# Optimization experiments

Measured on AMD Instinct MI355X. Metric: run time of the kernel, lower is better.

The kernel has to match this reference:

```python
import jax, jax.numpy as jnp
import numpy as np

B = 1024          # batch
X = 32 * 32       # x_neuron_num
Y = 16384         # y_neuron_num (codebook size)
Z = 1000          # z_neuron_num (classes)
P_BU = 0.5        # y_bottom_up_percent


def _l2n(a, axis):
    # F.normalize: x / max(||x||, 1e-12)
    return a / jnp.maximum(jnp.linalg.norm(a, axis=axis, keepdims=True), 1e-12)


def setup_inputs() -> dict:
    key = jax.random.key(0)
    ks = jax.random.split(key, 8)
    return {
        "x": jax.random.normal(ks[0], (B, 32, 32), jnp.float32),
        "z": jax.random.randint(ks[1], (B,), 0, Z),
        "x2y_w": jax.random.uniform(ks[2], (Y, X), jnp.float32),
        "z2y_w": jax.random.uniform(ks[3], (Y, Z), jnp.float32),
        "y2z_w": jax.random.uniform(ks[4], (Z, Y), jnp.float32),
        "y_age": jax.random.randint(ks[5], (1, Y), 0, 5).astype(jnp.float32),
        "z_age": jax.random.randint(ks[6], (1, Z), 0, 5).astype(jnp.float32),
        "y_threshold": jax.random.uniform(ks[7], (1, Y), jnp.float32) * 0.5,
        "per_item": 1,
    }


def reference(x, z, x2y_w, z2y_w, y2z_w, y_age, z_age, y_threshold, per_item):
    # one 'train' step (torch forward returns inside the per_item loop)
    batch = x.shape[0]
    x = _l2n(x.reshape(batch, -1), 1)                 # [B, X]
    z_hot = jax.nn.one_hot(z, Z, dtype=x.dtype)       # normalized one-hot == one-hot
    Wx = _l2n(x2y_w, 1)                               # [Y, X]
    Wz = _l2n(z2y_w, 1)                               # [Y, Z]
    U = _l2n(y2z_w, 1)                                # [Z, Y]

    y_pre = P_BU * (x @ Wx.T) + (1.0 - P_BU) * (z_hot @ Wz.T)  # [B, Y]

    age = y_age[0]
    thr = y_threshold[0]
    max_resp = jnp.max(y_pre, axis=1)                 # [B]
    max_idx = jnp.argmax(y_pre, axis=1)               # [B]
    # age/threshold tie-break: losers re-argmax over unactivated neurons
    judge = (max_resp > thr[max_idx]) | (age[max_idx] < 1.0)
    unact = (age < 1.0).astype(y_pre.dtype)           # [Y]
    any_unact = jnp.sum(unact) > 0
    fallback = jnp.argmax(y_pre * unact[None, :], axis=1)
    max_idx = jnp.where(judge | ~any_unact, max_idx, fallback)

    # --- Hebbian update of x2y / z2y, expressed as segment reductions ---
    # torch dense form: sum_b y_lr[b,j]*(inp[b]-W[j]) / divisor_j
    ones_b = jnp.ones((batch,), x.dtype)
    cnt = jax.ops.segment_sum(ones_b, max_idx, num_segments=Y)       # [Y]
    div = jnp.where(cnt > 0, cnt, 1.0)
    lr = 1.0 / (age + 1.0)                                           # [Y]
    sumx = jax.ops.segment_sum(x, max_idx, num_segments=Y)           # [Y, X]
    Wx_new = Wx + (lr[:, None] * (sumx - cnt[:, None] * Wx)) / div[:, None]
    sumz = jax.ops.segment_sum(z_hot, max_idx, num_segments=Y)       # [Y, Z]
    Wz_new = Wz + (lr[:, None] * (sumz - cnt[:, None] * Wz)) / div[:, None]
    age_new = age + cnt

    # --- threshold update: per-winner min response (3 for non-winners) ---
    seg_min = jax.ops.segment_min(max_resp, max_idx, num_segments=Y)
    y_cur = jnp.minimum(seg_min, 3.0)
    y_cur = jnp.where(y_cur > 2.0, 0.0, y_cur)
    y_lr_eff = jnp.where(cnt > 0, lr, 0.0)   # sum_b y_lr[b,j]/divisor_j
    thr_new = y_lr_eff * y_cur + (1.0 - y_lr_eff) * thr

    # --- y2z update, segmented by label z ---
    zage = z_age[0]
    zlr = 1.0 / (zage + 1.0)                                          # [Z]
    y_resp = jax.nn.one_hot(max_idx, Y, dtype=x.dtype)                # [B, Y]
    cz = jax.ops.segment_sum(ones_b, z, num_segments=Z)               # [Z]
    dz = jnp.where(cz > 0, cz, 1.0)
    sumy = jax.ops.segment_sum(y_resp, z, num_segments=Z)             # [Z, Y]
    U_new = U + (zlr[:, None] * (sumy - cz[:, None] * U)) / dz[:, None]
    zage_new = zage + cz

    y_activated_num = jnp.sum((age_new >= 1.0).astype(jnp.int32))
    return (y_activated_num, max_resp, Wx_new, Wz_new, U_new,
            thr_new[None, :], age_new[None, :], zage_new[None, :])
```

## Files before the change

### kernel.cpp

```cpp
#include <hip/hip_runtime.h>

#define B_N 1024
#define X_N 1024
#define Y_N 16384
#define Z_N 1000
#define GK  2048
#define MARGIN 0.004f

#define OFF_ACT      0
#define OFF_MAXRESP  1
#define OFF_WX       1025
#define OFF_WZ       16778241
#define OFF_U        33162241
#define OFF_THR      49546241
#define OFF_AGE      49562625
#define OFF_ZAGE     49579009

#define SCR_B_BYTES    4112ull
#define SCR_S_BYTES    67112992ull
#define SCR_A_BYTES    132648976ull
#define SCR_CAND_BYTES 136843296ull

#define WS_INV_X    0
#define WS_INV_WX   1024
#define WS_INV_WZ   17408
#define WS_FIDX     38912
#define WS_CNT      39936
#define WS_ZCNT     56320
#define WS_SEGMIN   57344
#define WS_CTR      73728
#define WS_MBITS    73736
#define WS_CCNT     74248

typedef unsigned short ushort_t;
typedef _Float16 f16x8 __attribute__((ext_vector_type(8)));
typedef float f32x4 __attribute__((ext_vector_type(4)));

__device__ __forceinline__ unsigned enc_f(float f) {
    unsigned u = __float_as_uint(f);
    return (u & 0x80000000u) ? ~u : (u | 0x80000000u);
}
__device__ __forceinline__ float dec_f(unsigned e) {
    unsigned u = (e & 0x80000000u) ? (e ^ 0x80000000u) : ~e;
    return __uint_as_float(u);
}
__device__ __forceinline__ unsigned long long pack_vi(float v, int y) {
    return ((unsigned long long)enc_f(v) << 32) |
           (unsigned long long)(0xFFFFFFFFu - (unsigned)y);
}
__device__ __forceinline__ ushort_t f2h(float f) {
    _Float16 h = (_Float16)f;
    ushort_t u; __builtin_memcpy(&u, &h, 2); return u;
}
__device__ __forceinline__ float h2f(unsigned lo16) {
    ushort_t u = (ushort_t)lo16; _Float16 h;
    __builtin_memcpy(&h, &u, 2); return (float)h;
}

#define GLOAD16(gp, lp) __builtin_amdgcn_global_load_lds( \
    (const __attribute__((address_space(1))) void*)(gp),  \
    (__attribute__((address_space(3))) void*)(lp), 16, 0, 0)

__global__ void init_kernel(int* cnt, unsigned* segmin, int* zcnt, int* ctr) {
    int i = blockIdx.x * 256 + threadIdx.x;
    if (i < Y_N) { cnt[i] = 0; segmin[i] = 0xFFFFFFFFu; }
    if (i < 1024) zcnt[i] = 0;
    if (i < 8) ctr[i] = (i == 2) ? 0x7FFFFFFF : 0;
}

__global__ void unact_kernel(const float* __restrict__ y_age, int* ctr,
                             unsigned long long* __restrict__ mbits) {
    int i = blockIdx.x * 256 + threadIdx.x;
    int a = (y_age[i] < 1.0f) ? 1 : 0;
    unsigned long long m = __ballot(a);
    int mi = a ? 0x7FFFFFFF : i;
    #pragma unroll
    for (int s = 32; s > 0; s >>= 1) mi = min(mi, __shfl_xor(mi, s, 64));
    if ((threadIdx.x & 63) == 0) {
        atomicAdd(ctr, (int)__popcll(m));
        mbits[i >> 6] = m;
        if (mi != 0x7FFFFFFF) atomicMin(&ctr[2], mi);
    }
}

__global__ __launch_bounds__(256) void pack_x_kernel(
    const float* __restrict__ x, const int* __restrict__ zlab,
    ushort_t* __restrict__ A, float* __restrict__ inv_x) {
    const int b = blockIdx.x, t = threadIdx.x;
    const int lane = t & 63, wid = t >> 6;
    float4 v = reinterpret_cast<const float4*>(x + (size_t)b * X_N)[t];
    float ss = v.x*v.x + v.y*v.y + v.z*v.z + v.w*v.w;
    #pragma unroll
    for (int s = 32; s > 0; s >>= 1) ss += __shfl_xor(ss, s, 64);
    __shared__ float red[4];
    if (lane == 0) red[wid] = ss;
    __syncthreads();
    float inv = 1.0f / fmaxf(sqrtf(red[0] + red[1] + red[2] + red[3]), 1e-12f);
    if (t == 0) inv_x[b] = inv;
    float h = 0.5f * inv;
    ushort_t o1[4] = { f2h(v.x*h), f2h(v.y*h), f2h(v.z*h), f2h(v.w*h) };
    *reinterpret_cast<uint2*>(A + (size_t)b * GK + t * 4) = *reinterpret_cast<uint2*>(o1);
    int zb = zlab[b];
    ushort_t o2[4] = { 0, 0, 0, 0 };
    int base = t * 4;
    if (zb >= base && zb < base + 4) o2[zb - base] = (ushort_t)0x3800;
    *reinterpret_cast<uint2*>(A + (size_t)b * GK + X_N + t * 4) = *reinterpret_cast<uint2*>(o2);
}

__global__ __launch_bounds__(256) void pack_w_kernel(
    const float* __restrict__ wxw, const float* __restrict__ wzw,
    ushort_t* __restrict__ Bm, float* __restrict__ inv_wx, float* __restrict__ inv_wz) {
    const int y = blockIdx.x, t = threadIdx.x;
    const int lane = t & 63, wid = t >> 6;
    float4 a = reinterpret_cast<const float4*>(wxw + (size_t)y * X_N)[t];
    float4 zv = make_float4(0.f, 0.f, 0.f, 0.f);
    if (t < 250) zv = reinterpret_cast<const float4*>(wzw + (size_t)y * Z_N)[t];
    float s1 = a.x*a.x + a.y*a.y + a.z*a.z + a.w*a.w;
    float s2 = zv.x*zv.x + zv.y*zv.y + zv.z*zv.z + zv.w*zv.w;
    #pragma unroll
    for (int s = 32; s > 0; s >>= 1) {
        s1 += __shfl_xor(s1, s, 64);
        s2 += __shfl_xor(s2, s, 64);
    }
    __shared__ float r1[4], r2[4];
    if (lane == 0) { r1[wid] = s1; r2[wid] = s2; }
    __syncthreads();
    float inv1 = 1.0f / fmaxf(sqrtf(r1[0] + r1[1] + r1[2] + r1[3]), 1e-12f);
    float inv2 = 1.0f / fmaxf(sqrtf(r2[0] + r2[1] + r2[2] + r2[3]), 1e-12f);
    ushort_t o1[4] = { f2h(a.x*inv1), f2h(a.y*inv1), f2h(a.z*inv1), f2h(a.w*inv1) };
    *reinterpret_cast<uint2*>(Bm + (size_t)y * GK + t * 4) = *reinterpret_cast<uint2*>(o1);
    ushort_t o2[4] = { 0, 0, 0, 0 };
    if (t < 250) { o2[0]=f2h(zv.x*inv2); o2[1]=f2h(zv.y*inv2); o2[2]=f2h(zv.z*inv2); o2[3]=f2h(zv.w*inv2); }
    *reinterpret_cast<uint2*>(Bm + (size_t)y * GK + X_N + t * 4) = *reinterpret_cast<uint2*>(o2);
    if (t == 0) { inv_wx[y] = inv1; inv_wz[y] = inv2; }
}

__global__ __launch_bounds__(512, 1) void mm256_kernel(const ushort_t* __restrict__ A,
                                                       const ushort_t* __restrict__ Bm,
                                                       ushort_t* __restrict__ S) {
    __shared__ __align__(16) _Float16 lds[4][2][1024][8];
    const int t = threadIdx.x;
    const int wid = t >> 6, lane = t & 63;
    const int bid = blockIdx.x;
    const int lb = (bid & 7) * 32 + (bid >> 3);
    const int mt = lb & 3, nt = lb >> 2;
    const int b0 = mt * 256, y0 = nt * 256;
    const int wr = wid >> 2, wc = wid & 3;
    const int r = lane & 15, gq = lane >> 4;
    const int NK = GK / 32;

    f32x4 acc[8][4];
    #pragma unroll
    for (int i = 0; i < 8; ++i)
        #pragma unroll
        for (int j = 0; j < 4; ++j) acc[i][j] = (f32x4){0.f, 0.f, 0.f, 0.f};

    auto stage = [&](int buf, int k0) {
        #pragma unroll
        for (int rr = 0; rr < 2; ++rr) {
            int s = rr * 512 + t;
            int row = s & 255, g = s >> 8;
            GLOAD16(A  + (size_t)(b0 + row) * GK + k0 + g * 8, &lds[buf][0][s][0]);
            GLOAD16(Bm + (size_t)(y0 + row) * GK + k0 + g * 8, &lds[buf][1][s][0]);
        }
    };

    stage(0, 0);
    stage(1, 32);
    stage(2, 64);
    asm volatile("s_waitcnt vmcnt(8)" ::: "memory");
    __builtin_amdgcn_s_barrier();
    asm volatile("" ::: "memory");

    for (int ks = 0; ks < NK; ++ks) {
        const int cur = ks & 3;
        f16x8 bF[4];
        #pragma unroll
        for (int nf = 0; nf < 4; ++nf)
            bF[nf] = *reinterpret_cast<const f16x8*>(
                &lds[cur][1][gq * 256 + wc * 64 + nf * 16 + r][0]);
        __builtin_amdgcn_s_setprio(1);
        #pragma unroll
        for (int mf = 0; mf < 8; ++mf) {
            f16x8 aF = *reinterpret_cast<const f16x8*>(
                &lds[cur][0][gq * 256 + wr * 128 + mf * 16 + r][0]);
            #pragma unroll
            for (int nf = 0; nf < 4; ++nf)
                acc[mf][nf] = __builtin_amdgcn_mfma_f32_16x16x32_f16(
                    aF, bF[nf], acc[mf][nf], 0, 0, 0);
        }
        __builtin_amdgcn_s_setprio(0);
        if (ks == NK - 1) break;

        __builtin_amdgcn_s_barrier();
        asm volatile("" ::: "memory");
        if (ks + 3 < NK) {
            stage((ks + 3) & 3, (ks + 3) * 32);
            asm volatile("s_waitcnt vmcnt(8)" ::: "memory");
        } else if (ks + 3 == NK) {
            asm volatile("s_waitcnt vmcnt(4)" ::: "memory");
        } else {
            asm volatile("s_waitcnt vmcnt(0)" ::: "memory");
        }
        __builtin_amdgcn_s_barrier();
        asm volatile("" ::: "memory");
    }

    #pragma unroll
    for (int mf = 0; mf < 8; ++mf) {
        int bg = b0 + wr * 128 + mf * 16 + gq * 4;
        #pragma unroll
        for (int nf = 0; nf < 4; ++nf) {
            int yg = y0 + wc * 64 + nf * 16 + r;
            f32x4 c = acc[mf][nf];
            #pragma unroll
            for (int q = 0; q < 4; ++q)
                S[(size_t)(bg + q) * Y_N + yg] = f2h(c[q]);
        }
    }
}

__global__ __launch_bounds__(256) void scan_kernel(
    const ushort_t* __restrict__ scores, const unsigned long long* __restrict__ mbits,
    const int* __restrict__ ctr, unsigned* __restrict__ gcand, int* __restrict__ ccnt) {
    const int b = blockIdx.x, t = threadIdx.x;
    const int lane = t & 63, wid = t >> 6;
    const uint4* srow = reinterpret_cast<const uint4*>(scores + (size_t)b * Y_N);

    float vmax = -1e30f, mmax = -1e30f;
    for (int c = t; c < Y_N / 8; c += 256) {
        uint4 pk = srow[c];
        int yb = c * 8;
        unsigned m8 = (unsigned)((mbits[yb >> 6] >> (yb & 63)) & 0xFFull);
        unsigned w[4] = {pk.x, pk.y, pk.z, pk.w};
        #pragma unroll
        for (int j = 0; j < 4; ++j) {
            float v0 = h2f(w[j] & 0xFFFFu);
            float v1 = h2f(w[j] >> 16);
            vmax = fmaxf(vmax, fmaxf(v0, v1));
            mmax = fmaxf(mmax, v0 * (float)((m8 >> (2 * j)) & 1u));
            mmax = fmaxf(mmax, v1 * (float)((m8 >> (2 * j + 1)) & 1u));
        }
    }
    #pragma unroll
    for (int s = 32; s > 0; s >>= 1) {
        vmax = fmaxf(vmax, __shfl_xor(vmax, s, 64));
        mmax = fmaxf(mmax, __shfl_xor(mmax, s, 64));
    }
    __shared__ float rv[4], rm[4];
    __shared__ int nA_s, nB_s;
    __shared__ int cA[256], cB[256];
    if (lane == 0) { rv[wid] = vmax; rm[wid] = mmax; }
    if (t == 0) { nA_s = 0; nB_s = 0; }
    __syncthreads();
    float tA = fmaxf(fmaxf(rv[0], rv[1]), fmaxf(rv[2], rv[3])) - MARGIN;
    float tB = fmaxf(fmaxf(rm[0], rm[1]), fmaxf(rm[2], rm[3])) - MARGIN;
    bool anyu = ctr[0] > 0;

    for (int c = t; c < Y_N / 8; c += 256) {
        uint4 pk = srow[c];
        int yb = c * 8;
        unsigned m8 = (unsigned)((mbits[yb >> 6] >> (yb & 63)) & 0xFFull);
        unsigned w[4] = {pk.x, pk.y, pk.z, pk.w};
        #pragma unroll
        for (int j = 0; j < 8; ++j) {
            float v = h2f((j & 1) ? (w[j >> 1] >> 16) : (w[j >> 1] & 0xFFFFu));
            if (v >= tA) { int p = atomicAdd(&nA_s, 1); if (p < 256) cA[p] = yb + j; }
            if (anyu && ((m8 >> j) & 1u) && v >= tB) {
                int p = atomicAdd(&nB_s, 1); if (p < 256) cB[p] = yb + j;
            }
        }
    }
    __syncthreads();
    int nA = min(nA_s, 256), nB = min(nB_s, 256);
    unsigned* slab = gcand + (size_t)b * 512;
    for (int i = t; i < nA; i += 256) slab[i] = (unsigned)cA[i];
    for (int i = t; i < nB; i += 256) slab[256 + i] = (unsigned)cB[i];
    if (t == 0) ccnt[b] = nA | (nB << 16);
}

__global__ __launch_bounds__(256) void rescore_kernel(
    const unsigned* __restrict__ gcand, const int* __restrict__ ccnt,
    const float* __restrict__ x, const float* __restrict__ inv_x,
    const float* __restrict__ wxw, const float* __restrict__ inv_wx,
    const float* __restrict__ wzw, const float* __restrict__ inv_wz,
    const int* __restrict__ zlab, const float* __restrict__ y_thr,
    const float* __restrict__ y_age, const int* __restrict__ ctr,
    int* final_idx, int* cnt, unsigned* segmin, int* zcnt,
    float* __restrict__ out_maxresp) {
    const int b = blockIdx.x, t = threadIdx.x;
    const int lane = t & 63, wid = t >> 6;
    int pc = ccnt[b];
    int nA = pc & 0xFFFF, nB = pc >> 16;
    int zb = zlab[b];
    float invx = inv_x[b];
    const unsigned* slab = gcand + (size_t)b * 512;

    const float4* xr = reinterpret_cast<const float4*>(x + (size_t)b * X_N);
    float4 xv[4];
    #pragma unroll
    for (int j = 0; j < 4; ++j) xv[j] = xr[j * 64 + lane];

    __shared__ unsigned long long red[4];
    __shared__ unsigned long long sPM;
    __shared__ int sTakeA;

    unsigned long long bA = 0ull;
    for (int c = wid; c < nA; c += 8) {
        int y1 = (int)slab[c];
        int c2 = c + 4;
        bool h2 = c2 < nA;
        int y2 = (int)slab[h2 ? c2 : c];
        const float4* w1 = reinterpret_cast<const float4*>(wxw + (size_t)y1 * X_N);
        const float4* w2 = reinterpret_cast<const float4*>(wxw + (size_t)y2 * X_N);
        float d1 = 0.f, d2 = 0.f;
        #pragma unroll
        for (int j = 0; j < 4; ++j) {
            float4 a1 = w1[j * 64 + lane];
            float4 a2 = w2[j * 64 + lane];
            d1 += xv[j].x*a1.x + xv[j].y*a1.y + xv[j].z*a1.z + xv[j].w*a1.w;
            d2 += xv[j].x*a2.x + xv[j].y*a2.y + xv[j].z*a2.z + xv[j].w*a2.w;
        }
        #pragma unroll
        for (int s = 32; s > 0; s >>= 1) {
            d1 += __shfl_xor(d1, s, 64);
            d2 += __shfl_xor(d2, s, 64);
        }
        float v1 = 0.5f*invx*inv_wx[y1]*d1 + 0.5f*inv_wz[y1]*wzw[(size_t)y1*Z_N + zb];
        unsigned long long p1 = pack_vi(v1, y1);
        bA = (p1 > bA) ? p1 : bA;
        if (h2) {
            float v2 = 0.5f*invx*inv_wx[y2]*d2 + 0.5f*inv_wz[y2]*wzw[(size_t)y2*Z_N + zb];
            unsigned long long p2 = pack_vi(v2, y2);
            bA = (p2 > bA) ? p2 : bA;
        }
    }
    if (lane == 0) red[wid] = bA;
    __syncthreads();
    if (t == 0) {
        unsigned long long pm = red[0];
        #pragma unroll
        for (int j = 1; j < 4; ++j) pm = (red[j] > pm) ? red[j] : pm;
        sPM = pm;
        unsigned enc = (unsigned)(pm >> 32);
        int idx = (int)(0xFFFFFFFFu - (unsigned)(pm & 0xFFFFFFFFull));
        float mresp = dec_f(enc);
        out_maxresp[b] = mresp;
        bool judge = (mresp > y_thr[idx]) || (y_age[idx] < 1.0f);
        bool anyu = ctr[0] > 0;
        sTakeA = (judge || !anyu) ? 1 : 0;
    }
    __syncthreads();

    if (!sTakeA) {
        unsigned long long bB = 0ull;
        for (int c = wid; c < nB; c += 8) {
            int y1 = (int)slab[256 + c];
            int c2 = c + 4;
            bool h2 = c2 < nB;
            int y2 = (int)slab[256 + (h2 ? c2 : c)];
            const float4* w1 = reinterpret_cast<const float4*>(wxw + (size_t)y1 * X_N);
            const float4* w2 = reinterpret_cast<const float4*>(wxw + (size_t)y2 * X_N);
            float d1 = 0.f, d2 = 0.f;
            #pragma unroll
            for (int j = 0; j < 4; ++j) {
                float4 a1 = w1[j * 64 + lane];
                float4 a2 = w2[j * 64 + lane];
                d1 += xv[j].x*a1.x + xv[j].y*a1.y + xv[j].z*a1.z + xv[j].w*a1.w;
                d2 += xv[j].x*a2.x + xv[j].y*a2.y + xv[j].z*a2.z + xv[j].w*a2.w;
            }
            #pragma unroll
            for (int s = 32; s > 0; s >>= 1) {
                d1 += __shfl_xor(d1, s, 64);
                d2 += __shfl_xor(d2, s, 64);
            }
            float v1 = 0.5f*invx*inv_wx[y1]*d1 + 0.5f*inv_wz[y1]*wzw[(size_t)y1*Z_N + zb];
            unsigned long long p1 = pack_vi(v1, y1);
            bB = (p1 > bB) ? p1 : bB;
            if (h2) {
                float v2 = 0.5f*invx*inv_wx[y2]*d2 + 0.5f*inv_wz[y2]*wzw[(size_t)y2*Z_N + zb];
                unsigned long long p2 = pack_vi(v2, y2);
                bB = (p2 > bB) ? p2 : bB;
            }
        }
        if (lane == 0) red[wid] = bB;
    }
    __syncthreads();
    if (t == 0) {
        unsigned long long pm = sPM;
        unsigned enc = (unsigned)(pm >> 32);
        int idx = (int)(0xFFFFFFFFu - (unsigned)(pm & 0xFFFFFFFFull));
        int fin;
        if (sTakeA) {
            fin = idx;
        } else if (nB > 0) {
            unsigned long long pf = red[0];
            #pragma unroll
            for (int j = 1; j < 4; ++j) pf = (red[j] > pf) ? red[j] : pf;
            fin = (int)(0xFFFFFFFFu - (unsigned)(pf & 0xFFFFFFFFull));
        } else {
            fin = ctr[2];
        }
        final_idx[b] = fin;
        atomicAdd(&cnt[fin], 1);
        atomicMin(&segmin[fin], enc);
        atomicAdd(&zcnt[zb], 1);
    }
}

__global__ __launch_bounds__(256) void wx_out_kernel(
    const float* __restrict__ wxw, const float* __restrict__ inv_wx,
    const float* __restrict__ x, const float* __restrict__ inv_x,
    const int* __restrict__ final_idx, const int* __restrict__ cnt,
    const float* __restrict__ y_age, float* __restrict__ outw) {
    int j = blockIdx.x;
    int t = threadIdx.x;
    __shared__ int s_b[1024];
    __shared__ int s_n;
    if (t == 0) s_n = 0;
    __syncthreads();
    int c = cnt[j];
    if (c > 0) {
        for (int b = t; b < B_N; b += 256)
            if (final_idx[b] == j) { int p = atomicAdd(&s_n, 1); s_b[p] = b; }
    }
    __syncthreads();
    float inv = inv_wx[j];
    float lr = 1.0f / (y_age[j] + 1.0f);
    float fc = (float)c;
    float dv = (c > 0) ? fc : 1.0f;
    int n = s_n;
    float4 w = *reinterpret_cast<const float4*>(wxw + (size_t)j * X_N + t * 4);
    float4 wn = make_float4(w.x*inv, w.y*inv, w.z*inv, w.w*inv);
    if (c > 0) {
        float4 s = make_float4(0.f, 0.f, 0.f, 0.f);
        for (int m = 0; m < n; ++m) {
            int b = s_b[m];
            float ix = inv_x[b];
            float4 xv = *reinterpret_cast<const float4*>(x + (size_t)b * X_N + t * 4);
            s.x += xv.x * ix; s.y += xv.y * ix; s.z += xv.z * ix; s.w += xv.w * ix;
        }
        float f = lr / dv;
        wn.x += f * (s.x - fc * wn.x);
        wn.y += f * (s.y - fc * wn.y);
        wn.z += f * (s.z - fc * wn.z);
        wn.w += f * (s.w - fc * wn.w);
    }
    *reinterpret_cast<float4*>(outw + (size_t)j * X_N + t * 4) = wn;
}

__global__ __launch_bounds__(256) void wz_out_kernel(
    const float* __restrict__ wzw, const float* __restrict__ inv_wz,
    const int* __restrict__ zlab, const int* __restrict__ final_idx,
    const int* __restrict__ cnt, const float* __restrict__ y_age,
    float* __restrict__ outw) {
    int j = blockIdx.x;
    int t = threadIdx.x;
    __shared__ int s_c[1024];
    __shared__ int s_n;
    if (t == 0) s_n = 0;
    __syncthreads();
    int c = cnt[j];
    if (c > 0) {
        for (int b = t; b < B_N; b += 256)
            if (final_idx[b] == j) { int p = atomicAdd(&s_n, 1); s_c[p] = zlab[b]; }
    }
    __syncthreads();
    if (t >= 250) return;
    float inv = inv_wz[j];
    float lr = 1.0f / (y_age[j] + 1.0f);
    float fc = (float)c;
    float dv = (c > 0) ? fc : 1.0f;
    int n = s_n;
    float4 w = *reinterpret_cast<const float4*>(wzw + (size_t)j * Z_N + t * 4);
    float4 wn = make_float4(w.x*inv, w.y*inv, w.z*inv, w.w*inv);
    if (c > 0) {
        float4 s = make_float4(0.f, 0.f, 0.f, 0.f);
        for (int m = 0; m < n; ++m) {
            int d = s_c[m] - t * 4;
            if (d == 0) s.x += 1.f;
            else if (d == 1) s.y += 1.f;
            else if (d == 2) s.z += 1.f;
            else if (d == 3) s.w += 1.f;
        }
        float f = lr / dv;
        wn.x += f * (s.x - fc * wn.x);
        wn.y += f * (s.y - fc * wn.y);
        wn.z += f * (s.z - fc * wn.z);
        wn.w += f * (s.w - fc * wn.w);
    }
    *reinterpret_cast<float4*>(outw + (size_t)j * Z_N + t * 4) = wn;
}

__global__ __launch_bounds__(256) void u_out_kernel(
    const float* __restrict__ uw, const int* __restrict__ zlab,
    const int* __restrict__ final_idx, const int* __restrict__ zcnt,
    const float* __restrict__ z_age, float* __restrict__ outw) {
    int cz = blockIdx.x;
    int t = threadIdx.x;
    const int lane = t & 63, wid = t >> 6;
    __shared__ int s_w[1024];
    __shared__ int s_n;
    __shared__ float rss[4];
    if (t == 0) s_n = 0;

    const float4* rowp4 = reinterpret_cast<const float4*>(uw + (size_t)cz * Y_N);
    float4 u[16];
    float ss = 0.f;
    #pragma unroll
    for (int p = 0; p < 16; ++p) {
        u[p] = rowp4[p * 256 + t];
        ss += u[p].x*u[p].x + u[p].y*u[p].y + u[p].z*u[p].z + u[p].w*u[p].w;
    }
    #pragma unroll
    for (int s = 32; s > 0; s >>= 1) ss += __shfl_xor(ss, s, 64);
    if (lane == 0) rss[wid] = ss;
    __syncthreads();
    float inv = 1.0f / fmaxf(sqrtf(rss[0] + rss[1] + rss[2] + rss[3]), 1e-12f);

    int c = zcnt[cz];
    if (c > 0) {
        for (int b = t; b < B_N; b += 256)
            if (zlab[b] == cz) { int p = atomicAdd(&s_n, 1); s_w[p] = final_idx[b]; }
    }
    __syncthreads();
    float zlr = 1.0f / (z_age[cz] + 1.0f);
    float fc = (float)c;
    float dv = (c > 0) ? fc : 1.0f;
    float f = zlr / dv;
    int n = s_n;
    float* outp = outw + (size_t)cz * Y_N;
    #pragma unroll
    for (int p = 0; p < 16; ++p) {
        int e4 = p * 256 + t;
        float4 un = make_float4(u[p].x*inv, u[p].y*inv, u[p].z*inv, u[p].w*inv);
        if (c > 0) {
            float4 s = make_float4(0.f, 0.f, 0.f, 0.f);
            for (int m = 0; m < n; ++m) {
                int d = s_w[m] - e4 * 4;
                if (d == 0) s.x += 1.f;
                else if (d == 1) s.y += 1.f;
                else if (d == 2) s.z += 1.f;
                else if (d == 3) s.w += 1.f;
            }
            un.x += f * (s.x - fc * un.x);
            un.y += f * (s.y - fc * un.y);
            un.z += f * (s.z - fc * un.z);
            un.w += f * (s.w - fc * un.w);
        }
        *reinterpret_cast<float4*>(outp + e4 * 4) = un;
    }
}

__global__ void thr_age_kernel(const int* __restrict__ cnt, const unsigned* __restrict__ segmin,
                               const float* __restrict__ y_age, const float* __restrict__ y_thr,
                               float* __restrict__ out_thr, float* __restrict__ out_age,
                               int* ctr) {
    int j = blockIdx.x * 256 + threadIdx.x;
    int c = cnt[j];
    float age = y_age[j];
    float thr = y_thr[j];
    float tn = thr;
    if (c > 0) {
        float lr = 1.0f / (age + 1.0f);
        float smin = dec_f(segmin[j]);
        float ycur = fminf(smin, 3.0f);
        if (ycur > 2.0f) ycur = 0.0f;
        tn = lr * ycur + (1.0f - lr) * thr;
    }
    out_thr[j] = tn;
    float an = age + (float)c;
    out_age[j] = an;
    unsigned long long m = __ballot(an >= 1.0f ? 1 : 0);
    if ((threadIdx.x & 63) == 0) atomicAdd(ctr + 1, (int)__popcll(m));
}

__global__ void zage_act_kernel(const int* __restrict__ zcnt, const float* __restrict__ z_age,
                                const int* __restrict__ ctr, float* __restrict__ out_zage,
                                float* __restrict__ out_act) {
    int i = blockIdx.x * 256 + threadIdx.x;
    if (i < Z_N) out_zage[i] = z_age[i] + (float)zcnt[i];
    if (i == 0) out_act[0] = (float)ctr[1];
}

extern "C" void kernel_launch(void* const* d_in, const int* in_sizes, int n_in,
                              void* d_out, int out_size, void* d_ws, size_t ws_size,
                              hipStream_t stream) {
    const float* x     = (const float*)d_in[0];
    const int*   z     = (const int*)d_in[1];
    const float* wxw   = (const float*)d_in[2];
    const float* wzw   = (const float*)d_in[3];
    const float* uw    = (const float*)d_in[4];
    const float* y_age = (const float*)d_in[5];
    const float* z_age = (const float*)d_in[6];
    const float* y_thr = (const float*)d_in[7];
    float* out = (float*)d_out;
    float* ws  = (float*)d_ws;
    char*  ob  = (char*)d_out;

    float* inv_x  = ws + WS_INV_X;
    float* inv_wx = ws + WS_INV_WX;
    float* inv_wz = ws + WS_INV_WZ;
    int* fidx = (int*)(ws + WS_FIDX);
    int* cnt  = (int*)(ws + WS_CNT);
    int* zcnt = (int*)(ws + WS_ZCNT);
    unsigned* segmin = (unsigned*)(ws + WS_SEGMIN);
    int* ctr = (int*)(ws + WS_CTR);
    unsigned long long* mbits = (unsigned long long*)(ws + WS_MBITS);
    int* ccnt = (int*)(ws + WS_CCNT);

    ushort_t* Bb = (ushort_t*)(ob + SCR_B_BYTES);
    ushort_t* Sc = (ushort_t*)(ob + SCR_S_BYTES);
    ushort_t* Ab = (ushort_t*)(ob + SCR_A_BYTES);
    unsigned* gcand = (unsigned*)(ob + SCR_CAND_BYTES);

    init_kernel<<<64, 256, 0, stream>>>(cnt, segmin, zcnt, ctr);
    unact_kernel<<<Y_N / 256, 256, 0, stream>>>(y_age, ctr, mbits);
    pack_x_kernel<<<B_N, 256, 0, stream>>>(x, z, Ab, inv_x);
    pack_w_kernel<<<Y_N, 256, 0, stream>>>(wxw, wzw, Bb, inv_wx, inv_wz);
    mm256_kernel<<<(B_N / 256) * (Y_N / 256), 512, 0, stream>>>(Ab, Bb, Sc);
    scan_kernel<<<B_N, 256, 0, stream>>>(Sc, mbits, ctr, gcand, ccnt);
    rescore_kernel<<<B_N, 256, 0, stream>>>(gcand, ccnt, x, inv_x, wxw, inv_wx, wzw, inv_wz,
                                            z, y_thr, y_age, ctr, fidx, cnt, segmin, zcnt,
                                            out + OFF_MAXRESP);
    wx_out_kernel<<<Y_N, 256, 0, stream>>>(wxw, inv_wx, x, inv_x, fidx, cnt, y_age, out + OFF_WX);
    wz_out_kernel<<<Y_N, 256, 0, stream>>>(wzw, inv_wz, z, fidx, cnt, y_age, out + OFF_WZ);
    u_out_kernel<<<Z_N, 256, 0, stream>>>(uw, z, fidx, zcnt, z_age, out + OFF_U);
    thr_age_kernel<<<Y_N / 256, 256, 0, stream>>>(cnt, segmin, y_age, y_thr,
                                                  out + OFF_THR, out + OFF_AGE, ctr);
    zage_act_kernel<<<4, 256, 0, stream>>>(zcnt, z_age, ctr, out + OFF_ZAGE, out + OFF_ACT);
}
```

Before: 289.7 us.

## Replace one-hot GEMM half with gathered transposed Wz row added in scan

The score GEMM previously concatenated the one-hot label into the K dimension (K=2048), which doubled the MMA work for the z term. It now runs the GEMM over only the x features (K=1024) and builds a transposed, pre-scaled fp16 copy of the normalized Wz. The scan kernel gathers the row for each sample's label and adds it to the scores. This halves GEMM FLOPs and operand traffic, at the cost of an extra transpose kernel and a second 32KB row read per sample in scan.

After: 259.0 us. -10.6%, faster.

```diff
diff --git a/kernel.cpp b/kernel.cpp
--- a/kernel.cpp
+++ b/kernel.cpp
@@ -4,7 +4,7 @@
 #define X_N 1024
 #define Y_N 16384
 #define Z_N 1000
-#define GK  2048
+#define KD  1024
 #define MARGIN 0.004f
 
 #define OFF_ACT      0
@@ -17,9 +17,10 @@
 #define OFF_ZAGE     49579009
 
 #define SCR_B_BYTES    4112ull
-#define SCR_S_BYTES    67112992ull
+#define SCR_S_BYTES    67112976ull
 #define SCR_A_BYTES    132648976ull
-#define SCR_CAND_BYTES 136843296ull
+#define SCR_CAND_BYTES 134746128ull
+#define SCR_WZT_BYTES  136843280ull
 
 #define WS_INV_X    0
 #define WS_INV_WX   1024
@@ -84,8 +85,7 @@
 }
 
 __global__ __launch_bounds__(256) void pack_x_kernel(
-    const float* __restrict__ x, const int* __restrict__ zlab,
-    ushort_t* __restrict__ A, float* __restrict__ inv_x) {
+    const float* __restrict__ x, ushort_t* __restrict__ A, float* __restrict__ inv_x) {
     const int b = blockIdx.x, t = threadIdx.x;
     const int lane = t & 63, wid = t >> 6;
     float4 v = reinterpret_cast<const float4*>(x + (size_t)b * X_N)[t];
@@ -97,14 +97,8 @@
     __syncthreads();
     float inv = 1.0f / fmaxf(sqrtf(red[0] + red[1] + red[2] + red[3]), 1e-12f);
     if (t == 0) inv_x[b] = inv;
-    float h = 0.5f * inv;
-    ushort_t o1[4] = { f2h(v.x*h), f2h(v.y*h), f2h(v.z*h), f2h(v.w*h) };
-    *reinterpret_cast<uint2*>(A + (size_t)b * GK + t * 4) = *reinterpret_cast<uint2*>(o1);
-    int zb = zlab[b];
-    ushort_t o2[4] = { 0, 0, 0, 0 };
-    int base = t * 4;
-    if (zb >= base && zb < base + 4) o2[zb - base] = (ushort_t)0x3800;
-    *reinterpret_cast<uint2*>(A + (size_t)b * GK + X_N + t * 4) = *reinterpret_cast<uint2*>(o2);
+    ushort_t o1[4] = { f2h(v.x*inv), f2h(v.y*inv), f2h(v.z*inv), f2h(v.w*inv) };
+    *reinterpret_cast<uint2*>(A + (size_t)b * KD + t * 4) = *reinterpret_cast<uint2*>(o1);
 }
 
 __global__ __launch_bounds__(256) void pack_w_kernel(
@@ -128,11 +122,42 @@
     float inv1 = 1.0f / fmaxf(sqrtf(r1[0] + r1[1] + r1[2] + r1[3]), 1e-12f);
     float inv2 = 1.0f / fmaxf(sqrtf(r2[0] + r2[1] + r2[2] + r2[3]), 1e-12f);
     ushort_t o1[4] = { f2h(a.x*inv1), f2h(a.y*inv1), f2h(a.z*inv1), f2h(a.w*inv1) };
-    *reinterpret_cast<uint2*>(Bm + (size_t)y * GK + t * 4) = *reinterpret_cast<uint2*>(o1);
-    ushort_t o2[4] = { 0, 0, 0, 0 };
-    if (t < 250) { o2[0]=f2h(zv.x*inv2); o2[1]=f2h(zv.y*inv2); o2[2]=f2h(zv.z*inv2); o2[3]=f2h(zv.w*inv2); }
-    *reinterpret_cast<uint2*>(Bm + (size_t)y * GK + X_N + t * 4) = *reinterpret_cast<uint2*>(o2);
+    *reinterpret_cast<uint2*>(Bm + (size_t)y * KD + t * 4) = *reinterpret_cast<uint2*>(o1);
     if (t == 0) { inv_wx[y] = inv1; inv_wz[y] = inv2; }
+}
+
+__global__ __launch_bounds__(256) void wzt_kernel(
+    const float* __restrict__ wzw, const float* __restrict__ inv_wz,
+    ushort_t* __restrict__ wzt) {
+    const int bid = blockIdx.x;
+    const int z0 = (bid & 15) * 64, y0 = (bid >> 4) * 64;
+    const int t = threadIdx.x;
+    __shared__ float tile[64][65];
+    #pragma unroll
+    for (int p = 0; p < 4; ++p) {
+        int yr = p * 16 + (t >> 4);
+        int z = z0 + (t & 15) * 4;
+        float4 v = make_float4(0.f, 0.f, 0.f, 0.f);
+        if (z + 3 < Z_N)
+            v = *reinterpret_cast<const float4*>(wzw + (size_t)(y0 + yr) * Z_N + z);
+        float s = 0.5f * inv_wz[y0 + yr];
+        tile[(t & 15) * 4 + 0][yr] = v.x * s;
+        tile[(t & 15) * 4 + 1][yr] = v.y * s;
+        tile[(t & 15) * 4 + 2][yr] = v.z * s;
+        tile[(t & 15) * 4 + 3][yr] = v.w * s;
+    }
+    __syncthreads();
+    #pragma unroll
+    for (int p = 0; p < 4; ++p) {
+        int zr = p * 16 + (t >> 4);
+        int yc = (t & 15) * 4;
+        if (z0 + zr < 1024) {
+            ushort_t o[4] = { f2h(tile[zr][yc]), f2h(tile[zr][yc + 1]),
+                              f2h(tile[zr][yc + 2]), f2h(tile[zr][yc + 3]) };
+            *reinterpret_cast<uint2*>(wzt + (size_t)(z0 + zr) * Y_N + y0 + yc) =
+                *reinterpret_cast<uint2*>(o);
+        }
+    }
 }
 
 __global__ __launch_bounds__(512, 1) void mm256_kernel(const ushort_t* __restrict__ A,
@@ -147,7 +172,7 @@
     const int b0 = mt * 256, y0 = nt * 256;
     const int wr = wid >> 2, wc = wid & 3;
     const int r = lane & 15, gq = lane >> 4;
-    const int NK = GK / 32;
+    const int NK = KD / 32;
 
     f32x4 acc[8][4];
     #pragma unroll
@@ -160,8 +185,8 @@
         for (int rr = 0; rr < 2; ++rr) {
             int s = rr * 512 + t;
             int row = s & 255, g = s >> 8;
-            GLOAD16(A  + (size_t)(b0 + row) * GK + k0 + g * 8, &lds[buf][0][s][0]);
-            GLOAD16(Bm + (size_t)(y0 + row) * GK + k0 + g * 8, &lds[buf][1][s][0]);
+            GLOAD16(A  + (size_t)(b0 + row) * KD + k0 + g * 8, &lds[buf][0][s][0]);
+            GLOAD16(Bm + (size_t)(y0 + row) * KD + k0 + g * 8, &lds[buf][1][s][0]);
         }
     };
 
@@ -215,28 +240,32 @@
             f32x4 c = acc[mf][nf];
             #pragma unroll
             for (int q = 0; q < 4; ++q)
-                S[(size_t)(bg + q) * Y_N + yg] = f2h(c[q]);
+                S[(size_t)(bg + q) * Y_N + yg] = f2h(0.5f * c[q]);
         }
     }
 }
 
 __global__ __launch_bounds__(256) void scan_kernel(
-    const ushort_t* __restrict__ scores, const unsigned long long* __restrict__ mbits,
+    const ushort_t* __restrict__ scores, const ushort_t* __restrict__ wzt,
+    const int* __restrict__ zlab, const unsigned long long* __restrict__ mbits,
     const int* __restrict__ ctr, unsigned* __restrict__ gcand, int* __restrict__ ccnt) {
     const int b = blockIdx.x, t = threadIdx.x;
     const int lane = t & 63, wid = t >> 6;
     const uint4* srow = reinterpret_cast<const uint4*>(scores + (size_t)b * Y_N);
+    const uint4* wrow = reinterpret_cast<const uint4*>(wzt + (size_t)zlab[b] * Y_N);
 
     float vmax = -1e30f, mmax = -1e30f;
     for (int c = t; c < Y_N / 8; c += 256) {
         uint4 pk = srow[c];
+        uint4 wz = wrow[c];
         int yb = c * 8;
         unsigned m8 = (unsigned)((mbits[yb >> 6] >> (yb & 63)) & 0xFFull);
         unsigned w[4] = {pk.x, pk.y, pk.z, pk.w};
+        unsigned q[4] = {wz.x, wz.y, wz.z, wz.w};
         #pragma unroll
         for (int j = 0; j < 4; ++j) {
-            float v0 = h2f(w[j] & 0xFFFFu);
-            float v1 = h2f(w[j] >> 16);
+            float v0 = h2f(w[j] & 0xFFFFu) + h2f(q[j] & 0xFFFFu);
+            float v1 = h2f(w[j] >> 16) + h2f(q[j] >> 16);
             vmax = fmaxf(vmax, fmaxf(v0, v1));
             mmax = fmaxf(mmax, v0 * (float)((m8 >> (2 * j)) & 1u));
             mmax = fmaxf(mmax, v1 * (float)((m8 >> (2 * j + 1)) & 1u));
@@ -259,12 +288,16 @@
 
     for (int c = t; c < Y_N / 8; c += 256) {
         uint4 pk = srow[c];
+        uint4 wz = wrow[c];
         int yb = c * 8;
         unsigned m8 = (unsigned)((mbits[yb >> 6] >> (yb & 63)) & 0xFFull);
         unsigned w[4] = {pk.x, pk.y, pk.z, pk.w};
+        unsigned q[4] = {wz.x, wz.y, wz.z, wz.w};
         #pragma unroll
         for (int j = 0; j < 8; ++j) {
-            float v = h2f((j & 1) ? (w[j >> 1] >> 16) : (w[j >> 1] & 0xFFFFu));
+            unsigned sw = (j & 1) ? (w[j >> 1] >> 16) : (w[j >> 1] & 0xFFFFu);
+            unsigned qw = (j & 1) ? (q[j >> 1] >> 16) : (q[j >> 1] & 0xFFFFu);
+            float v = h2f(sw) + h2f(qw);
             if (v >= tA) { int p = atomicAdd(&nA_s, 1); if (p < 256) cA[p] = yb + j; }
             if (anyu && ((m8 >> j) & 1u) && v >= tB) {
                 int p = atomicAdd(&nB_s, 1); if (p < 256) cB[p] = yb + j;
@@ -609,17 +642,19 @@
     unsigned long long* mbits = (unsigned long long*)(ws + WS_MBITS);
     int* ccnt = (int*)(ws + WS_CCNT);
 
-    ushort_t* Bb = (ushort_t*)(ob + SCR_B_BYTES);
-    ushort_t* Sc = (ushort_t*)(ob + SCR_S_BYTES);
-    ushort_t* Ab = (ushort_t*)(ob + SCR_A_BYTES);
+    ushort_t* Bb  = (ushort_t*)(ob + SCR_B_BYTES);
+    ushort_t* Sc  = (ushort_t*)(ob + SCR_S_BYTES);
+    ushort_t* Ab  = (ushort_t*)(ob + SCR_A_BYTES);
     unsigned* gcand = (unsigned*)(ob + SCR_CAND_BYTES);
+    ushort_t* wzt = (ushort_t*)(ob + SCR_WZT_BYTES);
 
     init_kernel<<<64, 256, 0, stream>>>(cnt, segmin, zcnt, ctr);
     unact_kernel<<<Y_N / 256, 256, 0, stream>>>(y_age, ctr, mbits);
-    pack_x_kernel<<<B_N, 256, 0, stream>>>(x, z, Ab, inv_x);
+    pack_x_kernel<<<B_N, 256, 0, stream>>>(x, Ab, inv_x);
     pack_w_kernel<<<Y_N, 256, 0, stream>>>(wxw, wzw, Bb, inv_wx, inv_wz);
+    wzt_kernel<<<16 * 256, 256, 0, stream>>>(wzw, inv_wz, wzt);
     mm256_kernel<<<(B_N / 256) * (Y_N / 256), 512, 0, stream>>>(Ab, Bb, Sc);
-    scan_kernel<<<B_N, 256, 0, stream>>>(Sc, mbits, ctr, gcand, ccnt);
+    scan_kernel<<<B_N, 256, 0, stream>>>(Sc, wzt, z, mbits, ctr, gcand, ccnt);
     rescore_kernel<<<B_N, 256, 0, stream>>>(gcand, ccnt, x, inv_x, wxw, inv_wx, wzw, inv_wz,
                                             z, y_thr, y_age, ctr, fidx, cnt, segmin, zcnt,
                                             out + OFF_MAXRESP);
```
